# Kernel optimization log

Measured on AMD Instinct MI355X. Metric: run time of the kernel, lower is better.

Reference implementation:

```python
import jax, jax.numpy as jnp
import numpy as np

EPS = 1e-5            # module's self.eps
DIST_EPS = 1e-8       # clamp on sqdist
ACOSH_EPS = 1e-7      # clamp arccosh arg to >= 1+eps
MAX_EUCLID_NORM = 32.0  # cap used by rescale_to_max_euclid (numeric safety before expmap)

# ---- Lorentz (hyperboloid, k=1) manifold ops ----

def l_inner(u, v, keepdims=False):
    # Minkowski inner product <u,v>_L = -u0*v0 + <u_s, v_s>
    p = u * v
    r = -p[..., 0] + p[..., 1:].sum(-1)
    return r[..., None] if keepdims else r

def centroid(x, axis=-2):
    # Lorentz centroid: normalize the (weighted) mean back onto the hyperboloid
    m = x.mean(axis)
    denom = jnp.sqrt(jnp.clip(-l_inner(m, m, keepdims=True), 1e-8))
    return m / denom

def sqdist(x, y):
    a = jnp.clip(-l_inner(x, y), 1.0 + ACOSH_EPS)
    d = jnp.arccosh(a)
    return d * d

def logmap(x, y):
    # log_x(y) = d(x,y) * (y + <x,y> x) / ||y + <x,y> x||_L
    xy = l_inner(x, y, keepdims=True)
    d = jnp.arccosh(jnp.clip(-xy, 1.0 + ACOSH_EPS))
    u = y + xy * x
    un = jnp.sqrt(jnp.clip(l_inner(u, u, keepdims=True), 1e-8))
    return d * u / un

def expmap(x, v):
    vn = jnp.sqrt(jnp.clip(l_inner(v, v, keepdims=True), 1e-8))
    return jnp.cosh(vn) * x + jnp.sinh(vn) * v / vn

def transp(x, y, v):
    # parallel transport of tangent v from x to y
    return v + l_inner(y, v, keepdims=True) / (1.0 - l_inner(x, y, keepdims=True)) * (x + y)

def rescale_to_max_euclid(v):
    n = jnp.linalg.norm(v, axis=-1, keepdims=True)
    return v * jnp.minimum(1.0, MAX_EUCLID_NORM / jnp.maximum(n, 1e-8))


def setup_inputs() -> dict:
    key = jax.random.key(0)
    k1, = jax.random.split(key, 1)
    B, T, D = 64, 1024, 256
    space = 0.5 * jax.random.normal(k1, (B, T, D - 1), dtype=jnp.float32)
    time = jnp.sqrt(1.0 + (space * space).sum(-1, keepdims=True))
    x = jnp.concatenate([time, space], axis=-1)  # points on hyperboloid
    beta = jnp.zeros((D,), dtype=jnp.float32).at[0].set(1.0)  # manifold origin
    gamma = jnp.ones((1,), dtype=jnp.float32)
    return {"x": x, "beta": beta, "gamma": gamma}


def reference(x, beta, gamma):
    # Training-path Lorentz batch norm (centroid mean + Frechet variance)
    mean = centroid(x)           # [B, D] (reduce tokens)
    mean = centroid(mean)        # [D]   (reduce batch)  -- 3D input path
    distances = jnp.clip(sqdist(x, mean), DIST_EPS)   # [B, T]
    x_T = logmap(mean, x)        # tangent at mean, [B, T, D]
    var = jnp.sqrt(distances.mean())                 # Frechet std (scalar)
    scale = gamma / (var + EPS)                      # [1]
    x_T = x_T * scale
    x_T = rescale_to_max_euclid(x_T)
    x_T = transp(mean, beta, x_T)
    out = expmap(beta, x_T)
    return out
```

## Files before the change

### kernel.cpp

```cpp
#include <hip/hip_runtime.h>
#include <hip/hip_fp16.h>
#include <math.h>

#define BB 64
#define TT 1024
#define DD 256
#define BT (BB*TT)
#define SS 16
#define TPC (TT/SS)

typedef float v4f __attribute__((ext_vector_type(4)));

#define PA_OFF   0
#define CENT_OFF (PA_OFF + 1024*DD)
#define MEAN_OFF (CENT_OFF + BB*DD)
#define SC_OFF   (MEAN_OFF + DD)
#define SCAL_OFF (SC_OFF + 16)
#define DP_OFF   (SCAL_OFF + BT*4)
#define XH_OFF   (DP_OFF + 1024)
#define WS_BYTES_NEEDED ((size_t)(XH_OFF)*4 + (size_t)BT*64*8)

__device__ __forceinline__ float block_reduce_256(float v) {
    __shared__ float sh[4];
    #pragma unroll
    for (int o = 32; o; o >>= 1) v += __shfl_xor(v, o, 64);
    int lane = threadIdx.x & 63, w = threadIdx.x >> 6;
    if (lane == 0) sh[w] = v;
    __syncthreads();
    float r = sh[0] + sh[1] + sh[2] + sh[3];
    __syncthreads();
    return r;
}

__device__ __forceinline__ ushort4 f4toh4(float4 v) {
    ushort4 r;
    r.x = __half_as_ushort(__float2half(v.x));
    r.y = __half_as_ushort(__float2half(v.y));
    r.z = __half_as_ushort(__float2half(v.z));
    r.w = __half_as_ushort(__float2half(v.w));
    return r;
}
__device__ __forceinline__ float4 h4tof4(ushort4 h) {
    float4 r;
    r.x = __half2float(__ushort_as_half(h.x));
    r.y = __half2float(__ushort_as_half(h.y));
    r.z = __half2float(__ushort_as_half(h.z));
    r.w = __half2float(__ushort_as_half(h.w));
    return r;
}

__global__ void kA_h(const float* __restrict__ x, float* __restrict__ ws,
                     ushort4* __restrict__ xh) {
    int tid = threadIdx.x, lane = tid & 63, wv = tid >> 6;
    int chunk = blockIdx.x;
    int tok0 = chunk * 64 + wv * 16;
    const float4* xp = (const float4*)x + (size_t)tok0 * 64 + lane;
    ushort4* hp = xh + (size_t)tok0 * 64 + lane;
    float4 s = {0.f, 0.f, 0.f, 0.f};
    #pragma unroll
    for (int t = 0; t < 16; ++t) {
        float4 v = xp[(size_t)t * 64];
        s.x += v.x; s.y += v.y; s.z += v.z; s.w += v.w;
        hp[(size_t)t * 64] = f4toh4(v);
    }
    __shared__ float4 sh4[4][64];
    sh4[wv][lane] = s;
    __syncthreads();
    if (wv == 0) {
        float4 a = sh4[0][lane], b = sh4[1][lane], c = sh4[2][lane], d = sh4[3][lane];
        a.x += b.x + c.x + d.x;
        a.y += b.y + c.y + d.y;
        a.z += b.z + c.z + d.z;
        a.w += b.w + c.w + d.w;
        ((float4*)(ws + PA_OFF + (size_t)chunk * DD))[lane] = a;
    }
}

__global__ void kA_f(const float* __restrict__ x, float* __restrict__ ws) {
    int tid = threadIdx.x, lane = tid & 63, wv = tid >> 6;
    int chunk = blockIdx.x;
    int tok0 = chunk * 64 + wv * 16;
    const float4* xp = (const float4*)x + (size_t)tok0 * 64 + lane;
    float4 s = {0.f, 0.f, 0.f, 0.f};
    #pragma unroll
    for (int t = 0; t < 16; ++t) {
        float4 v = xp[(size_t)t * 64];
        s.x += v.x; s.y += v.y; s.z += v.z; s.w += v.w;
    }
    __shared__ float4 sh4[4][64];
    sh4[wv][lane] = s;
    __syncthreads();
    if (wv == 0) {
        float4 a = sh4[0][lane], b = sh4[1][lane], c = sh4[2][lane], d = sh4[3][lane];
        a.x += b.x + c.x + d.x;
        a.y += b.y + c.y + d.y;
        a.z += b.z + c.z + d.z;
        a.w += b.w + c.w + d.w;
        ((float4*)(ws + PA_OFF + (size_t)chunk * DD))[lane] = a;
    }
}

__global__ void kB1(float* __restrict__ ws) {
    int b = blockIdx.x, d = threadIdx.x;
    float m = 0.f;
    #pragma unroll
    for (int s = 0; s < SS; ++s) m += ws[PA_OFF + (size_t)(b*SS + s) * DD + d];
    m *= (1.0f / TT);
    float dot = block_reduce_256(d == 0 ? -m*m : m*m);
    ws[CENT_OFF + (size_t)b * DD + d] = m / sqrtf(fmaxf(-dot, 1e-8f));
}

__global__ void kB2(const float* __restrict__ beta, float* __restrict__ ws) {
    int d = threadIdx.x;
    float a = 0.f;
    #pragma unroll 8
    for (int b = 0; b < BB; ++b) a += ws[CENT_OFF + (size_t)b * DD + d];
    a *= (1.0f / BB);
    float dot = block_reduce_256(d == 0 ? -a*a : a*a);
    float mean_d = a / sqrtf(fmaxf(-dot, 1e-8f));
    ws[MEAN_OFF + d] = mean_d;
    float bt = beta[d];
    float w_d = mean_d + bt;
    float mb  = block_reduce_256(d == 0 ? -mean_d*bt : mean_d*bt);
    float wwp = block_reduce_256(d == 0 ? -w_d*w_d : w_d*w_d);
    if (d == 0) {
        ws[SC_OFF + 1] = 1.0f / (1.0f - mb);
        ws[SC_OFF + 2] = mb;
        ws[SC_OFF + 3] = wwp;
        ws[SC_OFF + 4] = mean_d;
    }
}

__global__ void kC_h(const ushort4* __restrict__ xh, const float* __restrict__ beta,
                     float* __restrict__ ws) {
    int tid = threadIdx.x, lane = tid & 63, wv = tid >> 6;
    int g  = lane >> 4;
    int gl = lane & 15;

    float4 mc[4], bc[4];
    #pragma unroll
    for (int c = 0; c < 4; ++c) {
        mc[c] = ((const float4*)(ws + MEAN_OFF))[c * 16 + gl];
        bc[c] = ((const float4*)beta)[c * 16 + gl];
    }

    float lsum = 0.f;
    int tbase = blockIdx.x * 64 + wv * 16;
    #pragma unroll
    for (int it = 0; it < 4; ++it) {
        int tok = tbase + it * 4 + g;
        const ushort4* xq = xh + (size_t)tok * 64 + gl;
        float4 q0 = h4tof4(xq[0]),  q1 = h4tof4(xq[16]),
               q2 = h4tof4(xq[32]), q3 = h4tof4(xq[48]);

        float pxy = mc[0].x*q0.x + mc[0].y*q0.y + mc[0].z*q0.z + mc[0].w*q0.w
                  + mc[1].x*q1.x + mc[1].y*q1.y + mc[1].z*q1.z + mc[1].w*q1.w
                  + mc[2].x*q2.x + mc[2].y*q2.y + mc[2].z*q2.z + mc[2].w*q2.w
                  + mc[3].x*q3.x + mc[3].y*q3.y + mc[3].z*q3.z + mc[3].w*q3.w;
        float pby = bc[0].x*q0.x + bc[0].y*q0.y + bc[0].z*q0.z + bc[0].w*q0.w
                  + bc[1].x*q1.x + bc[1].y*q1.y + bc[1].z*q1.z + bc[1].w*q1.w
                  + bc[2].x*q2.x + bc[2].y*q2.y + bc[2].z*q2.z + bc[2].w*q2.w
                  + bc[3].x*q3.x + bc[3].y*q3.y + bc[3].z*q3.z + bc[3].w*q3.w;
        if (gl == 0) {
            pxy -= 2.0f * mc[0].x * q0.x;
            pby -= 2.0f * bc[0].x * q0.x;
        }
        #pragma unroll
        for (int o = 1; o < 16; o <<= 1) {
            pxy += __shfl_xor(pxy, o, 64);
            pby += __shfl_xor(pby, o, 64);
        }
        if (gl == 0) {
            float4 sc; sc.x = pxy; sc.y = pby; sc.z = q0.x; sc.w = 0.f;
            ((float4*)(ws + SCAL_OFF))[tok] = sc;
            float d = acoshf(fmaxf(-pxy, 1.0f + 1e-7f));
            lsum += fmaxf(d * d, 1e-8f);
        }
    }
    float tot = block_reduce_256(lsum);
    if (tid == 0) ws[DP_OFF + blockIdx.x] = tot;
}

__global__ void kC_f(const float* __restrict__ x, const float* __restrict__ beta,
                     float* __restrict__ ws) {
    int tid = threadIdx.x, lane = tid & 63, wv = tid >> 6;
    int g  = lane >> 4;
    int gl = lane & 15;
    float4 mc[4], bc[4];
    #pragma unroll
    for (int c = 0; c < 4; ++c) {
        mc[c] = ((const float4*)(ws + MEAN_OFF))[c * 16 + gl];
        bc[c] = ((const float4*)beta)[c * 16 + gl];
    }
    float lsum = 0.f;
    int tbase = blockIdx.x * 64 + wv * 16;
    #pragma unroll
    for (int it = 0; it < 4; ++it) {
        int tok = tbase + it * 4 + g;
        const float4* xq = (const float4*)(x + (size_t)tok * DD) + gl;
        float4 q0 = xq[0], q1 = xq[16], q2 = xq[32], q3 = xq[48];
        float pxy = mc[0].x*q0.x + mc[0].y*q0.y + mc[0].z*q0.z + mc[0].w*q0.w
                  + mc[1].x*q1.x + mc[1].y*q1.y + mc[1].z*q1.z + mc[1].w*q1.w
                  + mc[2].x*q2.x + mc[2].y*q2.y + mc[2].z*q2.z + mc[2].w*q2.w
                  + mc[3].x*q3.x + mc[3].y*q3.y + mc[3].z*q3.z + mc[3].w*q3.w;
        float pby = bc[0].x*q0.x + bc[0].y*q0.y + bc[0].z*q0.z + bc[0].w*q0.w
                  + bc[1].x*q1.x + bc[1].y*q1.y + bc[1].z*q1.z + bc[1].w*q1.w
                  + bc[2].x*q2.x + bc[2].y*q2.y + bc[2].z*q2.z + bc[2].w*q2.w
                  + bc[3].x*q3.x + bc[3].y*q3.y + bc[3].z*q3.z + bc[3].w*q3.w;
        if (gl == 0) {
            pxy -= 2.0f * mc[0].x * q0.x;
            pby -= 2.0f * bc[0].x * q0.x;
        }
        #pragma unroll
        for (int o = 1; o < 16; o <<= 1) {
            pxy += __shfl_xor(pxy, o, 64);
            pby += __shfl_xor(pby, o, 64);
        }
        if (gl == 0) {
            float4 sc; sc.x = pxy; sc.y = pby; sc.z = q0.x; sc.w = 0.f;
            ((float4*)(ws + SCAL_OFF))[tok] = sc;
            float d = acoshf(fmaxf(-pxy, 1.0f + 1e-7f));
            lsum += fmaxf(d * d, 1e-8f);
        }
    }
    float tot = block_reduce_256(lsum);
    if (tid == 0) ws[DP_OFF + blockIdx.x] = tot;
}

__global__ void kV(const float* __restrict__ gamma, float* __restrict__ ws) {
    int tid = threadIdx.x;
    float s = 0.f;
    #pragma unroll
    for (int i = tid; i < 1024; i += 256) s += ws[DP_OFF + i];
    float tot = block_reduce_256(s);
    if (tid == 0) {
        float var = sqrtf(tot / (float)BT);
        ws[SC_OFF + 0] = gamma[0] / (var + 1e-5f);
    }
}

__device__ __forceinline__ float4 abc_from_scal(float4 sc, float scale,
                                                float invden, float mb,
                                                float ww, float mean0) {
    float xy = sc.x, by = sc.y, y0 = sc.z;
    float d   = acoshf(fmaxf(-xy, 1.0f + 1e-7f));
    float un2 = fmaxf(xy * xy - 1.0f, 1e-8f);
    float f1  = d * scale / sqrtf(un2);
    float u0  = y0 + xy * mean0;
    float en2 = f1 * f1 * (un2 + 2.0f * u0 * u0);
    float n   = sqrtf(en2);
    float factor = fminf(1.0f, 32.0f / fmaxf(n, 1e-8f));
    float ff1 = factor * f1;
    float bv  = ff1 * (by + xy * mb);
    float coeff = bv * invden;
    float vn2 = ff1 * ff1 * un2 + 2.0f * coeff * bv + coeff * coeff * ww;
    float vn  = sqrtf(fmaxf(vn2, 1e-8f));
    float shv = sinhf(vn) / vn;
    float chv = coshf(vn);
    float4 abc;
    abc.x = shv * ff1;
    abc.y = shv * (ff1 * xy + coeff);
    abc.z = chv + shv * coeff;
    abc.w = 0.f;
    return abc;
}

__global__ void kE_h(const ushort4* __restrict__ xh, const float* __restrict__ beta,
                     const float* __restrict__ ws, float* __restrict__ out) {
    int tid = threadIdx.x, lane = tid & 63, wv = tid >> 6;
    int tok0 = blockIdx.x * 64;

    __shared__ float4 sabc[64];
    if (tid < 64) {
        float4 sc = ((const float4*)(ws + SCAL_OFF))[tok0 + tid];
        sabc[tid] = abc_from_scal(sc, ws[SC_OFF + 0], ws[SC_OFF + 1],
                                  ws[SC_OFF + 2], ws[SC_OFF + 3], ws[SC_OFF + 4]);
    }
    __syncthreads();

    float4 m4 = ((const float4*)(ws + MEAN_OFF))[lane];
    float4 b4 = ((const float4*)beta)[lane];
    const ushort4* xp = xh + (size_t)(tok0 + wv * 16) * 64 + lane;
    v4f* op = (v4f*)out + (size_t)(tok0 + wv * 16) * 64 + lane;

    #pragma unroll 4
    for (int t = 0; t < 16; ++t) {
        float4 abc = sabc[wv * 16 + t];
        float A = abc.x, B = abc.y, C = abc.z;
        float4 v = h4tof4(xp[(size_t)t * 64]);
        v4f o4;
        o4.x = A * v.x + B * m4.x + C * b4.x;
        o4.y = A * v.y + B * m4.y + C * b4.y;
        o4.z = A * v.z + B * m4.z + C * b4.z;
        o4.w = A * v.w + B * m4.w + C * b4.w;
        __builtin_nontemporal_store(o4, op + (size_t)t * 64);
    }
}

__global__ void kE_f(const float* __restrict__ x, const float* __restrict__ beta,
                     const float* __restrict__ ws, float* __restrict__ out) {
    int tid = threadIdx.x, lane = tid & 63, wv = tid >> 6;
    int tok0 = blockIdx.x * 64;

    __shared__ float4 sabc[64];
    if (tid < 64) {
        float4 sc = ((const float4*)(ws + SCAL_OFF))[tok0 + tid];
        sabc[tid] = abc_from_scal(sc, ws[SC_OFF + 0], ws[SC_OFF + 1],
                                  ws[SC_OFF + 2], ws[SC_OFF + 3], ws[SC_OFF + 4]);
    }
    __syncthreads();

    float4 m4 = ((const float4*)(ws + MEAN_OFF))[lane];
    float4 b4 = ((const float4*)beta)[lane];
    const float4* xp = (const float4*)x + (size_t)(tok0 + wv * 16) * 64 + lane;
    v4f* op = (v4f*)out + (size_t)(tok0 + wv * 16) * 64 + lane;

    #pragma unroll 4
    for (int t = 0; t < 16; ++t) {
        float4 abc = sabc[wv * 16 + t];
        float A = abc.x, B = abc.y, C = abc.z;
        float4 v = xp[(size_t)t * 64];
        v4f o4;
        o4.x = A * v.x + B * m4.x + C * b4.x;
        o4.y = A * v.y + B * m4.y + C * b4.y;
        o4.z = A * v.z + B * m4.z + C * b4.z;
        o4.w = A * v.w + B * m4.w + C * b4.w;
        __builtin_nontemporal_store(o4, op + (size_t)t * 64);
    }
}

extern "C" void kernel_launch(void* const* d_in, const int* in_sizes, int n_in,
                              void* d_out, int out_size, void* d_ws, size_t ws_size,
                              hipStream_t stream) {
    const float* x     = (const float*)d_in[0];
    const float* beta  = (const float*)d_in[1];
    const float* gamma = (const float*)d_in[2];
    float* out = (float*)d_out;
    float* ws  = (float*)d_ws;

    if (ws_size >= WS_BYTES_NEEDED) {
        ushort4* xh = (ushort4*)(ws + XH_OFF);
        kA_h<<<1024,  256, 0, stream>>>(x, ws, xh);
        kB1 <<<64,    256, 0, stream>>>(ws);
        kB2 <<<1,     256, 0, stream>>>(beta, ws);
        kC_h<<<1024,  256, 0, stream>>>(xh, beta, ws);
        kV  <<<1,     256, 0, stream>>>(gamma, ws);
        kE_h<<<BT/64, 256, 0, stream>>>(xh, beta, ws, out);
    } else {
        kA_f<<<1024,  256, 0, stream>>>(x, ws);
        kB1 <<<64,    256, 0, stream>>>(ws);
        kB2 <<<1,     256, 0, stream>>>(beta, ws);
        kC_f<<<1024,  256, 0, stream>>>(x, beta, ws);
        kV  <<<1,     256, 0, stream>>>(gamma, ws);
        kE_f<<<BT/64, 256, 0, stream>>>(x, beta, ws, out);
    }
}
```

Before: 56.34 us.

## Fold single-block mean and variance kernels into consumer kernel prologues

Removes the one-block kB2 and kV launches. Every kC block now recomputes the batch centroid from the per-batch centroids into shared memory, and block 0 publishes mean and scalars to the workspace. Every kE block redundantly reduces the 1024 partial distance sums to get the scale. This trades two launches and their serialization gaps for redundant per-block L2 reads: 64 KB of centroid data per kC block and 4 KB per kE block, plus extra reductions.

Measured after the change: 53.63 us. -4.8%, faster.

```diff
diff --git a/kernel.cpp b/kernel.cpp
--- a/kernel.cpp
+++ b/kernel.cpp
@@ -110,25 +110,29 @@
     ws[CENT_OFF + (size_t)b * DD + d] = m / sqrtf(fmaxf(-dot, 1e-8f));
 }
 
-__global__ void kB2(const float* __restrict__ beta, float* __restrict__ ws) {
-    int d = threadIdx.x;
+__device__ __forceinline__ float mean_prologue(const float* __restrict__ ws,
+                                               const float* __restrict__ beta,
+                                               float* smean, float* ssc) {
+    int tid = threadIdx.x;
     float a = 0.f;
     #pragma unroll 8
-    for (int b = 0; b < BB; ++b) a += ws[CENT_OFF + (size_t)b * DD + d];
+    for (int b = 0; b < BB; ++b) a += ws[CENT_OFF + (size_t)b * DD + tid];
     a *= (1.0f / BB);
-    float dot = block_reduce_256(d == 0 ? -a*a : a*a);
+    float dot = block_reduce_256(tid == 0 ? -a * a : a * a);
     float mean_d = a / sqrtf(fmaxf(-dot, 1e-8f));
-    ws[MEAN_OFF + d] = mean_d;
-    float bt = beta[d];
+    smean[tid] = mean_d;
+    float bt = beta[tid];
     float w_d = mean_d + bt;
-    float mb  = block_reduce_256(d == 0 ? -mean_d*bt : mean_d*bt);
-    float wwp = block_reduce_256(d == 0 ? -w_d*w_d : w_d*w_d);
-    if (d == 0) {
-        ws[SC_OFF + 1] = 1.0f / (1.0f - mb);
-        ws[SC_OFF + 2] = mb;
-        ws[SC_OFF + 3] = wwp;
-        ws[SC_OFF + 4] = mean_d;
-    }
+    float mb  = block_reduce_256(tid == 0 ? -mean_d * bt : mean_d * bt);
+    float wwp = block_reduce_256(tid == 0 ? -w_d * w_d : w_d * w_d);
+    if (tid == 0) {
+        ssc[0] = 1.0f / (1.0f - mb);
+        ssc[1] = mb;
+        ssc[2] = wwp;
+        ssc[3] = mean_d;
+    }
+    __syncthreads();
+    return mean_d;
 }
 
 __global__ void kC_h(const ushort4* __restrict__ xh, const float* __restrict__ beta,
@@ -137,10 +141,19 @@
     int g  = lane >> 4;
     int gl = lane & 15;
 
+    __shared__ float smean[DD];
+    __shared__ float ssc[4];
+    float mean_d = mean_prologue(ws, beta, smean, ssc);
+
+    if (blockIdx.x == 0) {
+        ws[MEAN_OFF + tid] = mean_d;
+        if (tid < 4) ws[SC_OFF + 1 + tid] = ssc[tid];
+    }
+
     float4 mc[4], bc[4];
     #pragma unroll
     for (int c = 0; c < 4; ++c) {
-        mc[c] = ((const float4*)(ws + MEAN_OFF))[c * 16 + gl];
+        mc[c] = ((const float4*)smean)[c * 16 + gl];
         bc[c] = ((const float4*)beta)[c * 16 + gl];
     }
 
@@ -186,10 +199,19 @@
     int tid = threadIdx.x, lane = tid & 63, wv = tid >> 6;
     int g  = lane >> 4;
     int gl = lane & 15;
+
+    __shared__ float smean[DD];
+    __shared__ float ssc[4];
+    float mean_d = mean_prologue(ws, beta, smean, ssc);
+    if (blockIdx.x == 0) {
+        ws[MEAN_OFF + tid] = mean_d;
+        if (tid < 4) ws[SC_OFF + 1 + tid] = ssc[tid];
+    }
+
     float4 mc[4], bc[4];
     #pragma unroll
     for (int c = 0; c < 4; ++c) {
-        mc[c] = ((const float4*)(ws + MEAN_OFF))[c * 16 + gl];
+        mc[c] = ((const float4*)smean)[c * 16 + gl];
         bc[c] = ((const float4*)beta)[c * 16 + gl];
     }
     float lsum = 0.f;
@@ -225,18 +247,6 @@
     }
     float tot = block_reduce_256(lsum);
     if (tid == 0) ws[DP_OFF + blockIdx.x] = tot;
-}
-
-__global__ void kV(const float* __restrict__ gamma, float* __restrict__ ws) {
-    int tid = threadIdx.x;
-    float s = 0.f;
-    #pragma unroll
-    for (int i = tid; i < 1024; i += 256) s += ws[DP_OFF + i];
-    float tot = block_reduce_256(s);
-    if (tid == 0) {
-        float var = sqrtf(tot / (float)BT);
-        ws[SC_OFF + 0] = gamma[0] / (var + 1e-5f);
-    }
 }
 
 __device__ __forceinline__ float4 abc_from_scal(float4 sc, float scale,
@@ -266,15 +276,23 @@
 }
 
 __global__ void kE_h(const ushort4* __restrict__ xh, const float* __restrict__ beta,
+                     const float* __restrict__ gamma,
                      const float* __restrict__ ws, float* __restrict__ out) {
     int tid = threadIdx.x, lane = tid & 63, wv = tid >> 6;
     int tok0 = blockIdx.x * 64;
+
+    float s = 0.f;
+    #pragma unroll
+    for (int i = tid; i < 1024; i += 256) s += ws[DP_OFF + i];
+    float tot = block_reduce_256(s);
+    float var = sqrtf(tot / (float)BT);
+    float scale = gamma[0] / (var + 1e-5f);
 
     __shared__ float4 sabc[64];
     if (tid < 64) {
         float4 sc = ((const float4*)(ws + SCAL_OFF))[tok0 + tid];
-        sabc[tid] = abc_from_scal(sc, ws[SC_OFF + 0], ws[SC_OFF + 1],
-                                  ws[SC_OFF + 2], ws[SC_OFF + 3], ws[SC_OFF + 4]);
+        sabc[tid] = abc_from_scal(sc, scale, ws[SC_OFF + 1], ws[SC_OFF + 2],
+                                  ws[SC_OFF + 3], ws[SC_OFF + 4]);
     }
     __syncthreads();
 
@@ -298,15 +316,23 @@
 }
 
 __global__ void kE_f(const float* __restrict__ x, const float* __restrict__ beta,
+                     const float* __restrict__ gamma,
                      const float* __restrict__ ws, float* __restrict__ out) {
     int tid = threadIdx.x, lane = tid & 63, wv = tid >> 6;
     int tok0 = blockIdx.x * 64;
+
+    float s = 0.f;
+    #pragma unroll
+    for (int i = tid; i < 1024; i += 256) s += ws[DP_OFF + i];
+    float tot = block_reduce_256(s);
+    float var = sqrtf(tot / (float)BT);
+    float scale = gamma[0] / (var + 1e-5f);
 
     __shared__ float4 sabc[64];
     if (tid < 64) {
         float4 sc = ((const float4*)(ws + SCAL_OFF))[tok0 + tid];
-        sabc[tid] = abc_from_scal(sc, ws[SC_OFF + 0], ws[SC_OFF + 1],
-                                  ws[SC_OFF + 2], ws[SC_OFF + 3], ws[SC_OFF + 4]);
+        sabc[tid] = abc_from_scal(sc, scale, ws[SC_OFF + 1], ws[SC_OFF + 2],
+                                  ws[SC_OFF + 3], ws[SC_OFF + 4]);
     }
     __syncthreads();
 
@@ -342,16 +368,12 @@
         ushort4* xh = (ushort4*)(ws + XH_OFF);
         kA_h<<<1024,  256, 0, stream>>>(x, ws, xh);
         kB1 <<<64,    256, 0, stream>>>(ws);
-        kB2 <<<1,     256, 0, stream>>>(beta, ws);
         kC_h<<<1024,  256, 0, stream>>>(xh, beta, ws);
-        kV  <<<1,     256, 0, stream>>>(gamma, ws);
-        kE_h<<<BT/64, 256, 0, stream>>>(xh, beta, ws, out);
+        kE_h<<<BT/64, 256, 0, stream>>>(xh, beta, gamma, ws, out);
     } else {
         kA_f<<<1024,  256, 0, stream>>>(x, ws);
         kB1 <<<64,    256, 0, stream>>>(ws);
-        kB2 <<<1,     256, 0, stream>>>(beta, ws);
         kC_f<<<1024,  256, 0, stream>>>(x, beta, ws);
-        kV  <<<1,     256, 0, stream>>>(gamma, ws);
-        kE_f<<<BT/64, 256, 0, stream>>>(x, beta, ws, out);
-    }
-}
+        kE_f<<<BT/64, 256, 0, stream>>>(x, beta, gamma, ws, out);
+    }
+}
```
